# Kernel optimization log

Hardware: AMD Instinct MI355X
Metric: run time of the kernel (lower is better)

## Reference

```python
import jax, jax.numpy as jnp
import numpy as np

B, N, D_IN = 64, 512, 768
FEA, HEADS = 256, 8
NEG_SLOPE = 0.2  # GATConv default leaky_relu slope


def setup_inputs() -> dict:
    key = jax.random.key(0)
    ks = jax.random.split(key, 7)
    scale = lambda fan_in: 1.0 / np.sqrt(fan_in)
    return {
        "x": jax.random.normal(ks[0], (B, N, D_IN), dtype=jnp.float32),
        # outer LazyLinear(fea_dim) with bias
        "W1": jax.random.normal(ks[1], (D_IN, FEA), dtype=jnp.float32) * scale(D_IN),
        "b1": jnp.zeros((FEA,), dtype=jnp.float32),
        # GATConv lin: Linear(FEA, HEADS*FEA, bias=False)
        "Wg": jax.random.normal(ks[2], (FEA, HEADS * FEA), dtype=jnp.float32) * scale(FEA),
        "att_src": jax.random.normal(ks[3], (HEADS, FEA), dtype=jnp.float32) * scale(FEA),
        "att_dst": jax.random.normal(ks[4], (HEADS, FEA), dtype=jnp.float32) * scale(FEA),
        # GATConv bias (concat=False -> out_channels)
        "bias_g": jnp.zeros((FEA,), dtype=jnp.float32),
    }


def reference(x, W1, b1, Wg, att_src, att_dst, bias_g):
    # outer projection: [B,N,FEA]
    x1 = jnp.einsum("bnd,df->bnf", x, W1) + b1
    # GAT projection into heads: [B,N,H,C]
    h = jnp.einsum("bnf,fk->bnk", x1, Wg).reshape(B, N, HEADS, FEA)
    # per-node attention logits: [B,N,H]
    a_src = jnp.einsum("bnhc,hc->bnh", h, att_src)
    a_dst = jnp.einsum("bnhc,hc->bnh", h, att_dst)
    # graph is fully connected + self-loops (PyG add_self_loops=True),
    # so per-target softmax == dense softmax over all source nodes j.
    # logits[b,h,i,j] = a_dst[b,i,h] + a_src[b,j,h]
    logits = a_dst.transpose(0, 2, 1)[:, :, :, None] + a_src.transpose(0, 2, 1)[:, :, None, :]
    logits = jnp.where(logits >= 0, logits, NEG_SLOPE * logits)  # leaky_relu
    alpha = jax.nn.softmax(logits, axis=-1)  # [B,H,I,J]
    # weighted aggregation: out[b,i,h,c] = sum_j alpha[b,h,i,j] * h[b,j,h,c]
    out = jnp.einsum("bhij,bjhc->bihc", alpha, h)
    out = out.mean(axis=2) + bias_g  # concat=False -> mean over heads, [B,N,FEA]
    return out.mean(axis=1)  # mean over nodes -> [B,FEA]
```

## Files before the change

kernel.cpp:

```cpp
#include <hip/hip_runtime.h>

#define BATCH 64
#define NNODE 512
#define D_IN 768
#define FEA 256
#define HEADS 8
#define M_ROWS (BATCH * NNODE)
#define NEG_SLOPE 0.2f
#define LOG2E 1.4426950408889634f
#define JC 16

typedef __attribute__((ext_vector_type(4))) float f32x4;
typedef __attribute__((ext_vector_type(8))) short bf16x8;

__device__ __forceinline__ ushort f2bf(float f) {
    union { float f; unsigned u; } v; v.f = f;
    unsigned r = v.u + 0x7fffu + ((v.u >> 16) & 1u);
    return (ushort)(r >> 16);
}
__device__ __forceinline__ float exp2fast(float v) { return __builtin_amdgcn_exp2f(v); }

__global__ __launch_bounds__(256) void k_att_proj(const float* __restrict__ Wg,
                                                  const float* __restrict__ att_src,
                                                  const float* __restrict__ att_dst,
                                                  float* __restrict__ was,
                                                  float* __restrict__ wad) {
    int h = blockIdx.x;
    const float* a = (blockIdx.y == 0) ? att_src : att_dst;
    float* o = (blockIdx.y == 0) ? was : wad;
    int wv = threadIdx.x >> 6, lane = threadIdx.x & 63;
    float4 av = *(const float4*)&a[h * FEA + lane * 4];
    int fbase = blockIdx.z * 64 + wv;
    #pragma unroll
    for (int i = 0; i < 16; i++) {
        int f = fbase + i * 4;
        float4 g = *(const float4*)&Wg[(size_t)f * (HEADS * FEA) + h * FEA + lane * 4];
        float p = g.x * av.x + g.y * av.y + g.z * av.z + g.w * av.w;
        #pragma unroll
        for (int off = 32; off; off >>= 1) p += __shfl_xor(p, off);
        if (lane == 0) o[h * FEA + f] = p;
    }
}

__global__ __launch_bounds__(256) void k_prep_was1(const float* __restrict__ W1,
                                                   const float* __restrict__ b1,
                                                   const float* __restrict__ was,
                                                   const float* __restrict__ wad,
                                                   ushort* __restrict__ Bpk,
                                                   float* __restrict__ c_sd) {
    __shared__ float wvl[16 * 260];
    __shared__ float w1l[8][256];
    __shared__ float partial[256];
    int t = threadIdx.x;
    int blk = blockIdx.x;
    int k0 = blk * 8;
    for (int i = t; i < 4096; i += 256) {
        int col = i >> 8, f = i & 255;
        wvl[col * 260 + f] = (col < 8) ? was[col * 256 + f] : wad[(col - 8) * 256 + f];
    }
    for (int i = t; i < 2048; i += 256) {
        int r = i >> 8, c = i & 255;
        w1l[r][c] = W1[(size_t)(k0 + r) * 256 + c];
    }
    __syncthreads();
    int col = t & 15, r = (t >> 4) & 7, half = t >> 7;
    float acc = 0.f;
    const float* wr = &w1l[r][half * 128];
    const float* vr = &wvl[col * 260 + half * 128];
    #pragma unroll 4
    for (int f0 = 0; f0 < 128; f0 += 4) {
        float4 a4 = *(const float4*)&wr[f0];
        float4 v4 = *(const float4*)&vr[f0];
        acc += a4.x * v4.x + a4.y * v4.y + a4.z * v4.z + a4.w * v4.w;
    }
    partial[t] = acc;
    __syncthreads();
    if (t < 128) {
        float tot = partial[t] + partial[t + 128];
        int kt = blk >> 2;
        int kloc = (blk & 3) * 8 + r;
        Bpk[kt * 1024 + ((kloc >> 3) * 16 + col) * 8 + (kloc & 7)] = f2bf(tot);
    }
    if (blk == 0 && t < 16) {
        float a = 0.f;
        for (int f = 0; f < 256; f++) a += b1[f] * wvl[t * 260 + f];
        c_sd[t] = a;
    }
}

__global__ __launch_bounds__(256) void k_logits(const float* __restrict__ x,
                                                const ushort* __restrict__ Bpk,
                                                const float* __restrict__ c_sd,
                                                float* __restrict__ a_src,
                                                float* __restrict__ a_dst) {
    int t = threadIdx.x;
    int w = t >> 6, l = t & 63;
    int lr = l & 15, lk = l >> 4;
    int row0w = blockIdx.x * 64 + w * 16;
    const float* ap = x + (size_t)(row0w + lr) * D_IN + lk * 8;
    const ushort* bp = Bpk + l * 8;

    f32x4 A0[3], A1[3];
    bf16x8 Bf[3];
    A0[0] = *(const f32x4*)(ap);      A1[0] = *(const f32x4*)(ap + 4);
    Bf[0] = *(const bf16x8*)(bp);
    A0[1] = *(const f32x4*)(ap + 32); A1[1] = *(const f32x4*)(ap + 36);
    Bf[1] = *(const bf16x8*)(bp + 1024);
    f32x4 acc = {};

    #pragma unroll
    for (int kt = 0; kt < 24; kt++) {
        int cur = kt % 3;
        if (kt + 2 < 24) {
            int nx = (kt + 2) % 3;
            A0[nx] = *(const f32x4*)(ap + (kt + 2) * 32);
            A1[nx] = *(const f32x4*)(ap + (kt + 2) * 32 + 4);
            Bf[nx] = *(const bf16x8*)(bp + (size_t)(kt + 2) * 1024);
        }
        bf16x8 af;
        af[0] = (short)f2bf(A0[cur].x); af[1] = (short)f2bf(A0[cur].y);
        af[2] = (short)f2bf(A0[cur].z); af[3] = (short)f2bf(A0[cur].w);
        af[4] = (short)f2bf(A1[cur].x); af[5] = (short)f2bf(A1[cur].y);
        af[6] = (short)f2bf(A1[cur].z); af[7] = (short)f2bf(A1[cur].w);
        acc = __builtin_amdgcn_mfma_f32_16x16x32_bf16(af, Bf[cur], acc, 0, 0, 0);
    }
    int col = lr;
    float cadd = c_sd[col];
    float* dst = (col < 8) ? a_src : a_dst;
    int h = col & 7;
    #pragma unroll
    for (int r = 0; r < 4; r++) {
        int rr = row0w + lk * 4 + r;
        int b = rr >> 9, n = rr & 511;
        dst[((size_t)(b * 8 + h) << 9) + n] = (acc[r] + cadd) * LOG2E;
    }
}

__global__ __launch_bounds__(512) void k_softmax(const float* __restrict__ a_src,
                                                 const float* __restrict__ a_dst,
                                                 float* __restrict__ wout,
                                                 float* __restrict__ s_w) {
    __shared__ float s_srt[512], d_srt[512];
    __shared__ float E1[512], E2[512], PA[512], PB[512];
    __shared__ float red[8], tA[8], tB[8];
    int t = threadIdx.x;
    int lane = t & 63, wv = t >> 6;
    int bh = blockIdx.x;
    float sv = a_src[((size_t)bh << 9) + t];
    float dv = a_dst[((size_t)bh << 9) + t];
    float v_s = sv, v_d = dv;
    float mx = sv;
    #pragma unroll
    for (int off = 32; off; off >>= 1) mx = fmaxf(mx, __shfl_xor(mx, off));
    if (lane == 0) red[wv] = mx;
    __syncthreads();
    mx = red[0];
    #pragma unroll
    for (int k = 1; k < 8; k++) mx = fmaxf(mx, red[k]);
    for (int k = 2; k <= 512; k <<= 1) {
        for (int j = k >> 1; j > 0; j >>= 1) {
            bool lower = ((t & j) == 0);
            bool tmin = (lower == ((t & k) == 0));
            if (j >= 64) {
                __syncthreads();
                s_srt[t] = v_s; d_srt[t] = v_d;
                __syncthreads();
                float ps = s_srt[t ^ j], pd = d_srt[t ^ j];
                v_s = tmin ? fminf(v_s, ps) : fmaxf(v_s, ps);
                v_d = tmin ? fminf(v_d, pd) : fmaxf(v_d, pd);
            } else {
                float ps = __shfl_xor(v_s, j);
                float pd = __shfl_xor(v_d, j);
                v_s = tmin ? fminf(v_s, ps) : fmaxf(v_s, ps);
                v_d = tmin ? fminf(v_d, pd) : fmaxf(v_d, pd);
            }
        }
    }
    __syncthreads();
    s_srt[t] = v_s; d_srt[t] = v_d;
    float e1 = exp2fast(v_s - mx);
    float e2 = exp2fast(0.2f * (v_s - mx));
    #pragma unroll
    for (int off = 1; off < 64; off <<= 1) {
        float u1 = __shfl_up(e1, off);
        float u2 = __shfl_up(e2, off);
        if (lane >= off) { e1 += u1; e2 += u2; }
    }
    if (lane == 63) { tA[wv] = e1; tB[wv] = e2; }
    __syncthreads();
    float pre1 = 0.f, pre2 = 0.f, tot1 = 0.f, tot2 = 0.f;
    #pragma unroll
    for (int k = 0; k < 8; k++) {
        float a = tA[k], b = tB[k];
        tot1 += a; tot2 += b;
        if (k < wv) { pre1 += a; pre2 += b; }
    }
    e1 += pre1; e2 += pre2;
    E1[t] = e1; E2[t] = e2;
    __syncthreads();
    float v = v_d + mx;
    float mi = fmaxf(v, NEG_SLOPE * v);
    float key = -v_d;
    int lo = 0, hi = 512;
    #pragma unroll
    for (int it = 0; it < 9; it++) {
        if (lo < hi) {
            int mid = (lo + hi) >> 1;
            if (s_srt[mid] < key) lo = mid + 1; else hi = mid;
        }
    }
    float e1pre = lo ? E1[lo - 1] : 0.f;
    float e2pre = lo ? E2[lo - 1] : 0.f;
    float ga = exp2fast(v - mi);
    float gb = exp2fast(0.2f * v - mi);
    float L = ga * (tot1 - e1pre) + gb * e2pre;
    float linv = 1.f / L;
    float pa = ga * linv, pb = gb * linv;
    #pragma unroll
    for (int off = 1; off < 64; off <<= 1) {
        float u1 = __shfl_up(pa, off);
        float u2 = __shfl_up(pb, off);
        if (lane >= off) { pa += u1; pb += u2; }
    }
    __syncthreads();
    if (lane == 63) { tA[wv] = pa; tB[wv] = pb; }
    __syncthreads();
    float prp1 = 0.f, prp2 = 0.f, totp1 = 0.f, totp2 = 0.f;
    #pragma unroll
    for (int k = 0; k < 8; k++) {
        float a = tA[k], b = tB[k];
        totp1 += a; totp2 += b;
        if (k < wv) { prp1 += a; prp2 += b; }
    }
    pa += prp1; pb += prp2;
    PA[t] = pa; PB[t] = pb;
    __syncthreads();
    float key2 = -sv;
    int lo2 = 0, hi2 = 512;
    #pragma unroll
    for (int it = 0; it < 9; it++) {
        if (lo2 < hi2) {
            int mid = (lo2 + hi2) >> 1;
            if (d_srt[mid] < key2) lo2 = mid + 1; else hi2 = mid;
        }
    }
    float papre = lo2 ? PA[lo2 - 1] : 0.f;
    float pbpre = lo2 ? PB[lo2 - 1] : 0.f;
    float e1j = exp2fast(sv - mx);
    float e2j = exp2fast(0.2f * (sv - mx));
    float wj = e1j * (totp1 - papre) + e2j * pbpre;
    wout[((size_t)bh << 9) + t] = wj;
    float ssum = wj;
    #pragma unroll
    for (int off = 32; off; off >>= 1) ssum += __shfl_xor(ssum, off);
    __syncthreads();
    if (lane == 0) red[wv] = ssum;
    __syncthreads();
    if (t == 0) {
        float a = 0.f;
        #pragma unroll
        for (int k = 0; k < 8; k++) a += red[k];
        s_w[bh] = a;
    }
}

__global__ __launch_bounds__(192) void k_zsum(const float* __restrict__ w,
                                              const float* __restrict__ x,
                                              float* __restrict__ z_part) {
    __shared__ float wl[256];
    int t = threadIdx.x;
    int b = blockIdx.x, jc = blockIdx.y;
    for (int i = t; i < 256; i += 192) {
        int h = i >> 5, j = i & 31;
        wl[i] = w[((size_t)(b * 8 + h) << 9) + jc * 32 + j];
    }
    __syncthreads();
    f32x4 acc[8] = {};
    const float* xp = x + ((size_t)(b * 512 + jc * 32)) * D_IN + t * 4;
    for (int j = 0; j < 32; j++) {
        f32x4 xv = *(const f32x4*)(xp + (size_t)j * D_IN);
        #pragma unroll
        for (int h = 0; h < 8; h++) {
            float wv = wl[h * 32 + j];
            acc[h] = acc[h] + wv * xv;
        }
    }
    #pragma unroll
    for (int h = 0; h < 8; h++)
        *(f32x4*)&z_part[((size_t)((b * JC + jc) * 8 + h)) * D_IN + t * 4] = acc[h];
}

__global__ __launch_bounds__(256) void k_y(const float* __restrict__ z_part,
                                           const float* __restrict__ W1,
                                           const float* __restrict__ b1,
                                           const float* __restrict__ s_w,
                                           float* __restrict__ y_part) {
    __shared__ float zl[8 * 196];
    int t = threadIdx.x;
    int b = blockIdx.x, ds = blockIdx.y;
    for (int sIdx = t; sIdx < 1536; sIdx += 256) {
        int k = sIdx / 192, dd = sIdx - k * 192;
        float v = 0.f;
        #pragma unroll
        for (int jc = 0; jc < JC; jc++)
            v += z_part[((size_t)((b * JC + jc) * 8 + k)) * D_IN + ds * 192 + dd];
        zl[k * 196 + dd] = v;
    }
    __syncthreads();
    float acc[8] = {};
    for (int dq = 0; dq < 48; dq++) {
        int dbase = ds * 192 + dq * 4;
        float w0 = W1[(size_t)(dbase + 0) * 256 + t];
        float w1 = W1[(size_t)(dbase + 1) * 256 + t];
        float w2 = W1[(size_t)(dbase + 2) * 256 + t];
        float w3 = W1[(size_t)(dbase + 3) * 256 + t];
        #pragma unroll
        for (int k = 0; k < 8; k++) {
            float4 zq = *(const float4*)&zl[k * 196 + dq * 4];
            acc[k] += zq.x * w0 + zq.y * w1 + zq.z * w2 + zq.w * w3;
        }
    }
    #pragma unroll
    for (int k = 0; k < 8; k++) {
        float v = acc[k];
        if (ds == 0) v += s_w[b * 8 + k] * b1[t];
        y_part[((size_t)ds * 512 + b * 8 + k) * 256 + t] = v;
    }
}

__global__ __launch_bounds__(256) void k_out(const float* __restrict__ y_part,
                                             const float* __restrict__ Wg,
                                             float* __restrict__ out_part) {
    __shared__ float Yl[64][16];
    int t = threadIdx.x;
    int h = blockIdx.x, fs = blockIdx.y, bq = blockIdx.z;
    int f0 = fs * 64, b0 = bq * 16;
    for (int sIdx = t; sIdx < 1024; sIdx += 256) {
        int bl = sIdx >> 6, fl = sIdx & 63;
        float v = 0.f;
        #pragma unroll
        for (int ds = 0; ds < 4; ds++)
            v += y_part[((size_t)(ds * 512) + (b0 + bl) * 8 + h) * 256 + f0 + fl];
        Yl[fl][bl] = v;
    }
    __syncthreads();
    float acc[16] = {};
    for (int fl = 0; fl < 64; fl++) {
        float wv = Wg[(size_t)(f0 + fl) * 2048 + h * 256 + t];
        #pragma unroll
        for (int bl = 0; bl < 16; bl++) acc[bl] += Yl[fl][bl] * wv;
    }
    #pragma unroll
    for (int bl = 0; bl < 16; bl++)
        out_part[((size_t)(h * 4 + fs) * 64 + b0 + bl) * 256 + t] = acc[bl];
}

__global__ __launch_bounds__(256) void k_out2(const float* __restrict__ out_part,
                                              const float* __restrict__ bias_g,
                                              float* __restrict__ out) {
    int t = threadIdx.x, b = blockIdx.x;
    float acc = 0.f;
    #pragma unroll
    for (int k = 0; k < 32; k++) acc += out_part[((size_t)k * 64 + b) * 256 + t];
    out[b * 256 + t] = bias_g[t] + acc * (1.f / 4096.f);
}

extern "C" void kernel_launch(void* const* d_in, const int* in_sizes, int n_in,
                              void* d_out, int out_size, void* d_ws, size_t ws_size,
                              hipStream_t stream) {
    const float* x       = (const float*)d_in[0];
    const float* W1      = (const float*)d_in[1];
    const float* b1      = (const float*)d_in[2];
    const float* Wg      = (const float*)d_in[3];
    const float* att_src = (const float*)d_in[4];
    const float* att_dst = (const float*)d_in[5];
    const float* bias_g  = (const float*)d_in[6];
    float* out = (float*)d_out;

    float* ws       = (float*)d_ws;
    float* was      = ws;
    float* wad      = ws + 2048;
    float* c_sd     = ws + 4096;
    ushort* Bpk     = (ushort*)(ws + 4112);
    float* a_src    = ws + 16400;
    float* a_dst    = ws + 278544;
    float* wsum     = ws + 540688;
    float* s_w      = ws + 802832;
    float* z_part   = ws + 803344;
    float* y_part   = ws + 7094800;
    float* out_part = ws + 7619088;

    k_att_proj<<<dim3(HEADS, 2, 4), 256, 0, stream>>>(Wg, att_src, att_dst, was, wad);
    k_prep_was1<<<96, 256, 0, stream>>>(W1, b1, was, wad, Bpk, c_sd);
    k_logits<<<M_ROWS / 64, 256, 0, stream>>>(x, Bpk, c_sd, a_src, a_dst);
    k_softmax<<<BATCH * HEADS, 512, 0, stream>>>(a_src, a_dst, wsum, s_w);
    k_zsum<<<dim3(BATCH, JC), 192, 0, stream>>>(wsum, x, z_part);
    k_y<<<dim3(BATCH, 4), 256, 0, stream>>>(z_part, W1, b1, s_w, y_part);
    k_out<<<dim3(HEADS, 4, 4), 256, 0, stream>>>(y_part, Wg, out_part);
    k_out2<<<BATCH, 256, 0, stream>>>(out_part, bias_g, out);
}
```

Baseline: 94.40 us.

## Fuse all eight stages into one cooperative persistent kernel with grid syncs

Replaces the eight separate kernel launches with a single cooperative kernel of 256 blocks of 512 threads. Stages are separated by grid.sync, and each block handles two former 256-thread work units or two softmax rows. The z-sum stage is repartitioned from 16 chunks to 4 per batch, with an in-block reduction, which shrinks the z_part buffer. This removes launch gaps and inter-kernel drain, at the cost of grid-wide barriers and idle blocks in the small stages.

```diff
diff --git a/kernel.cpp b/kernel.cpp
--- a/kernel.cpp
+++ b/kernel.cpp
@@ -1,14 +1,10 @@
 #include <hip/hip_runtime.h>
-
-#define BATCH 64
-#define NNODE 512
-#define D_IN 768
-#define FEA 256
-#define HEADS 8
-#define M_ROWS (BATCH * NNODE)
+#include <hip/hip_cooperative_groups.h>
+
+namespace cg = cooperative_groups;
+
 #define NEG_SLOPE 0.2f
 #define LOG2E 1.4426950408889634f
-#define JC 16
 
 typedef __attribute__((ext_vector_type(4))) float f32x4;
 typedef __attribute__((ext_vector_type(8))) short bf16x8;
@@ -20,349 +16,408 @@
 }
 __device__ __forceinline__ float exp2fast(float v) { return __builtin_amdgcn_exp2f(v); }
 
-__global__ __launch_bounds__(256) void k_att_proj(const float* __restrict__ Wg,
-                                                  const float* __restrict__ att_src,
-                                                  const float* __restrict__ att_dst,
-                                                  float* __restrict__ was,
-                                                  float* __restrict__ wad) {
-    int h = blockIdx.x;
-    const float* a = (blockIdx.y == 0) ? att_src : att_dst;
-    float* o = (blockIdx.y == 0) ? was : wad;
-    int wv = threadIdx.x >> 6, lane = threadIdx.x & 63;
-    float4 av = *(const float4*)&a[h * FEA + lane * 4];
-    int fbase = blockIdx.z * 64 + wv;
-    #pragma unroll
-    for (int i = 0; i < 16; i++) {
-        int f = fbase + i * 4;
-        float4 g = *(const float4*)&Wg[(size_t)f * (HEADS * FEA) + h * FEA + lane * 4];
-        float p = g.x * av.x + g.y * av.y + g.z * av.z + g.w * av.w;
-        #pragma unroll
-        for (int off = 32; off; off >>= 1) p += __shfl_xor(p, off);
-        if (lane == 0) o[h * FEA + f] = p;
-    }
-}
-
-__global__ __launch_bounds__(256) void k_prep_was1(const float* __restrict__ W1,
-                                                   const float* __restrict__ b1,
-                                                   const float* __restrict__ was,
-                                                   const float* __restrict__ wad,
-                                                   ushort* __restrict__ Bpk,
-                                                   float* __restrict__ c_sd) {
-    __shared__ float wvl[16 * 260];
-    __shared__ float w1l[8][256];
-    __shared__ float partial[256];
-    int t = threadIdx.x;
-    int blk = blockIdx.x;
-    int k0 = blk * 8;
-    for (int i = t; i < 4096; i += 256) {
-        int col = i >> 8, f = i & 255;
-        wvl[col * 260 + f] = (col < 8) ? was[col * 256 + f] : wad[(col - 8) * 256 + f];
-    }
-    for (int i = t; i < 2048; i += 256) {
-        int r = i >> 8, c = i & 255;
-        w1l[r][c] = W1[(size_t)(k0 + r) * 256 + c];
-    }
-    __syncthreads();
-    int col = t & 15, r = (t >> 4) & 7, half = t >> 7;
-    float acc = 0.f;
-    const float* wr = &w1l[r][half * 128];
-    const float* vr = &wvl[col * 260 + half * 128];
-    #pragma unroll 4
-    for (int f0 = 0; f0 < 128; f0 += 4) {
-        float4 a4 = *(const float4*)&wr[f0];
-        float4 v4 = *(const float4*)&vr[f0];
-        acc += a4.x * v4.x + a4.y * v4.y + a4.z * v4.z + a4.w * v4.w;
-    }
-    partial[t] = acc;
-    __syncthreads();
-    if (t < 128) {
-        float tot = partial[t] + partial[t + 128];
-        int kt = blk >> 2;
-        int kloc = (blk & 3) * 8 + r;
-        Bpk[kt * 1024 + ((kloc >> 3) * 16 + col) * 8 + (kloc & 7)] = f2bf(tot);
-    }
-    if (blk == 0 && t < 16) {
-        float a = 0.f;
-        for (int f = 0; f < 256; f++) a += b1[f] * wvl[t * 260 + f];
-        c_sd[t] = a;
-    }
-}
-
-__global__ __launch_bounds__(256) void k_logits(const float* __restrict__ x,
-                                                const ushort* __restrict__ Bpk,
-                                                const float* __restrict__ c_sd,
-                                                float* __restrict__ a_src,
-                                                float* __restrict__ a_dst) {
-    int t = threadIdx.x;
-    int w = t >> 6, l = t & 63;
-    int lr = l & 15, lk = l >> 4;
-    int row0w = blockIdx.x * 64 + w * 16;
-    const float* ap = x + (size_t)(row0w + lr) * D_IN + lk * 8;
-    const ushort* bp = Bpk + l * 8;
-
-    f32x4 A0[3], A1[3];
-    bf16x8 Bf[3];
-    A0[0] = *(const f32x4*)(ap);      A1[0] = *(const f32x4*)(ap + 4);
-    Bf[0] = *(const bf16x8*)(bp);
-    A0[1] = *(const f32x4*)(ap + 32); A1[1] = *(const f32x4*)(ap + 36);
-    Bf[1] = *(const bf16x8*)(bp + 1024);
-    f32x4 acc = {};
-
-    #pragma unroll
-    for (int kt = 0; kt < 24; kt++) {
-        int cur = kt % 3;
-        if (kt + 2 < 24) {
-            int nx = (kt + 2) % 3;
-            A0[nx] = *(const f32x4*)(ap + (kt + 2) * 32);
-            A1[nx] = *(const f32x4*)(ap + (kt + 2) * 32 + 4);
-            Bf[nx] = *(const bf16x8*)(bp + (size_t)(kt + 2) * 1024);
-        }
-        bf16x8 af;
-        af[0] = (short)f2bf(A0[cur].x); af[1] = (short)f2bf(A0[cur].y);
-        af[2] = (short)f2bf(A0[cur].z); af[3] = (short)f2bf(A0[cur].w);
-        af[4] = (short)f2bf(A1[cur].x); af[5] = (short)f2bf(A1[cur].y);
-        af[6] = (short)f2bf(A1[cur].z); af[7] = (short)f2bf(A1[cur].w);
-        acc = __builtin_amdgcn_mfma_f32_16x16x32_bf16(af, Bf[cur], acc, 0, 0, 0);
-    }
-    int col = lr;
-    float cadd = c_sd[col];
-    float* dst = (col < 8) ? a_src : a_dst;
-    int h = col & 7;
-    #pragma unroll
-    for (int r = 0; r < 4; r++) {
-        int rr = row0w + lk * 4 + r;
-        int b = rr >> 9, n = rr & 511;
-        dst[((size_t)(b * 8 + h) << 9) + n] = (acc[r] + cadd) * LOG2E;
-    }
-}
-
-__global__ __launch_bounds__(512) void k_softmax(const float* __restrict__ a_src,
-                                                 const float* __restrict__ a_dst,
-                                                 float* __restrict__ wout,
-                                                 float* __restrict__ s_w) {
-    __shared__ float s_srt[512], d_srt[512];
-    __shared__ float E1[512], E2[512], PA[512], PB[512];
-    __shared__ float red[8], tA[8], tB[8];
-    int t = threadIdx.x;
-    int lane = t & 63, wv = t >> 6;
-    int bh = blockIdx.x;
-    float sv = a_src[((size_t)bh << 9) + t];
-    float dv = a_dst[((size_t)bh << 9) + t];
-    float v_s = sv, v_d = dv;
-    float mx = sv;
-    #pragma unroll
-    for (int off = 32; off; off >>= 1) mx = fmaxf(mx, __shfl_xor(mx, off));
-    if (lane == 0) red[wv] = mx;
-    __syncthreads();
-    mx = red[0];
-    #pragma unroll
-    for (int k = 1; k < 8; k++) mx = fmaxf(mx, red[k]);
-    for (int k = 2; k <= 512; k <<= 1) {
-        for (int j = k >> 1; j > 0; j >>= 1) {
-            bool lower = ((t & j) == 0);
-            bool tmin = (lower == ((t & k) == 0));
-            if (j >= 64) {
-                __syncthreads();
-                s_srt[t] = v_s; d_srt[t] = v_d;
-                __syncthreads();
-                float ps = s_srt[t ^ j], pd = d_srt[t ^ j];
-                v_s = tmin ? fminf(v_s, ps) : fmaxf(v_s, ps);
-                v_d = tmin ? fminf(v_d, pd) : fmaxf(v_d, pd);
-            } else {
-                float ps = __shfl_xor(v_s, j);
-                float pd = __shfl_xor(v_d, j);
-                v_s = tmin ? fminf(v_s, ps) : fmaxf(v_s, ps);
-                v_d = tmin ? fminf(v_d, pd) : fmaxf(v_d, pd);
-            }
-        }
-    }
-    __syncthreads();
-    s_srt[t] = v_s; d_srt[t] = v_d;
-    float e1 = exp2fast(v_s - mx);
-    float e2 = exp2fast(0.2f * (v_s - mx));
-    #pragma unroll
-    for (int off = 1; off < 64; off <<= 1) {
-        float u1 = __shfl_up(e1, off);
-        float u2 = __shfl_up(e2, off);
-        if (lane >= off) { e1 += u1; e2 += u2; }
-    }
-    if (lane == 63) { tA[wv] = e1; tB[wv] = e2; }
-    __syncthreads();
-    float pre1 = 0.f, pre2 = 0.f, tot1 = 0.f, tot2 = 0.f;
-    #pragma unroll
-    for (int k = 0; k < 8; k++) {
-        float a = tA[k], b = tB[k];
-        tot1 += a; tot2 += b;
-        if (k < wv) { pre1 += a; pre2 += b; }
-    }
-    e1 += pre1; e2 += pre2;
-    E1[t] = e1; E2[t] = e2;
-    __syncthreads();
-    float v = v_d + mx;
-    float mi = fmaxf(v, NEG_SLOPE * v);
-    float key = -v_d;
-    int lo = 0, hi = 512;
-    #pragma unroll
-    for (int it = 0; it < 9; it++) {
-        if (lo < hi) {
-            int mid = (lo + hi) >> 1;
-            if (s_srt[mid] < key) lo = mid + 1; else hi = mid;
-        }
-    }
-    float e1pre = lo ? E1[lo - 1] : 0.f;
-    float e2pre = lo ? E2[lo - 1] : 0.f;
-    float ga = exp2fast(v - mi);
-    float gb = exp2fast(0.2f * v - mi);
-    float L = ga * (tot1 - e1pre) + gb * e2pre;
-    float linv = 1.f / L;
-    float pa = ga * linv, pb = gb * linv;
-    #pragma unroll
-    for (int off = 1; off < 64; off <<= 1) {
-        float u1 = __shfl_up(pa, off);
-        float u2 = __shfl_up(pb, off);
-        if (lane >= off) { pa += u1; pb += u2; }
-    }
-    __syncthreads();
-    if (lane == 63) { tA[wv] = pa; tB[wv] = pb; }
-    __syncthreads();
-    float prp1 = 0.f, prp2 = 0.f, totp1 = 0.f, totp2 = 0.f;
-    #pragma unroll
-    for (int k = 0; k < 8; k++) {
-        float a = tA[k], b = tB[k];
-        totp1 += a; totp2 += b;
-        if (k < wv) { prp1 += a; prp2 += b; }
-    }
-    pa += prp1; pb += prp2;
-    PA[t] = pa; PB[t] = pb;
-    __syncthreads();
-    float key2 = -sv;
-    int lo2 = 0, hi2 = 512;
-    #pragma unroll
-    for (int it = 0; it < 9; it++) {
-        if (lo2 < hi2) {
-            int mid = (lo2 + hi2) >> 1;
-            if (d_srt[mid] < key2) lo2 = mid + 1; else hi2 = mid;
-        }
-    }
-    float papre = lo2 ? PA[lo2 - 1] : 0.f;
-    float pbpre = lo2 ? PB[lo2 - 1] : 0.f;
-    float e1j = exp2fast(sv - mx);
-    float e2j = exp2fast(0.2f * (sv - mx));
-    float wj = e1j * (totp1 - papre) + e2j * pbpre;
-    wout[((size_t)bh << 9) + t] = wj;
-    float ssum = wj;
-    #pragma unroll
-    for (int off = 32; off; off >>= 1) ssum += __shfl_xor(ssum, off);
-    __syncthreads();
-    if (lane == 0) red[wv] = ssum;
-    __syncthreads();
-    if (t == 0) {
-        float a = 0.f;
-        #pragma unroll
-        for (int k = 0; k < 8; k++) a += red[k];
-        s_w[bh] = a;
-    }
-}
-
-__global__ __launch_bounds__(192) void k_zsum(const float* __restrict__ w,
-                                              const float* __restrict__ x,
-                                              float* __restrict__ z_part) {
-    __shared__ float wl[256];
-    int t = threadIdx.x;
-    int b = blockIdx.x, jc = blockIdx.y;
-    for (int i = t; i < 256; i += 192) {
-        int h = i >> 5, j = i & 31;
-        wl[i] = w[((size_t)(b * 8 + h) << 9) + jc * 32 + j];
-    }
-    __syncthreads();
-    f32x4 acc[8] = {};
-    const float* xp = x + ((size_t)(b * 512 + jc * 32)) * D_IN + t * 4;
-    for (int j = 0; j < 32; j++) {
-        f32x4 xv = *(const f32x4*)(xp + (size_t)j * D_IN);
-        #pragma unroll
-        for (int h = 0; h < 8; h++) {
-            float wv = wl[h * 32 + j];
-            acc[h] = acc[h] + wv * xv;
-        }
-    }
-    #pragma unroll
-    for (int h = 0; h < 8; h++)
-        *(f32x4*)&z_part[((size_t)((b * JC + jc) * 8 + h)) * D_IN + t * 4] = acc[h];
-}
-
-__global__ __launch_bounds__(256) void k_y(const float* __restrict__ z_part,
-                                           const float* __restrict__ W1,
-                                           const float* __restrict__ b1,
-                                           const float* __restrict__ s_w,
-                                           float* __restrict__ y_part) {
-    __shared__ float zl[8 * 196];
-    int t = threadIdx.x;
-    int b = blockIdx.x, ds = blockIdx.y;
-    for (int sIdx = t; sIdx < 1536; sIdx += 256) {
-        int k = sIdx / 192, dd = sIdx - k * 192;
-        float v = 0.f;
-        #pragma unroll
-        for (int jc = 0; jc < JC; jc++)
-            v += z_part[((size_t)((b * JC + jc) * 8 + k)) * D_IN + ds * 192 + dd];
-        zl[k * 196 + dd] = v;
-    }
-    __syncthreads();
-    float acc[8] = {};
-    for (int dq = 0; dq < 48; dq++) {
-        int dbase = ds * 192 + dq * 4;
-        float w0 = W1[(size_t)(dbase + 0) * 256 + t];
-        float w1 = W1[(size_t)(dbase + 1) * 256 + t];
-        float w2 = W1[(size_t)(dbase + 2) * 256 + t];
-        float w3 = W1[(size_t)(dbase + 3) * 256 + t];
+__global__ __launch_bounds__(512) void k_mega(
+    const float* __restrict__ x, const float* __restrict__ W1, const float* __restrict__ b1,
+    const float* __restrict__ Wg, const float* __restrict__ att_src, const float* __restrict__ att_dst,
+    const float* __restrict__ bias_g, float* __restrict__ out,
+    float* __restrict__ was, float* __restrict__ wad, float* __restrict__ c_sd,
+    ushort* __restrict__ Bpk, float* __restrict__ a_src, float* __restrict__ a_dst,
+    float* __restrict__ wsum, float* __restrict__ s_w, float* __restrict__ z_part,
+    float* __restrict__ y_part, float* __restrict__ out_part)
+{
+    __shared__ float smem[12928];
+    cg::grid_group grid = cg::this_grid();
+    const int t = threadIdx.x;
+    const int blk = blockIdx.x;
+    const int half = t >> 8;
+    const int tl = t & 255;
+
+    if (blk < 32) {
+        int u = blk * 2 + half;
+        int h = u & 7;
+        const float* a = ((u >> 3) & 1) ? att_dst : att_src;
+        float* o = ((u >> 3) & 1) ? wad : was;
+        int z4 = u >> 4;
+        int wv = tl >> 6, lane = tl & 63;
+        float4 av = *(const float4*)&a[h * 256 + lane * 4];
+        int fbase = z4 * 64 + wv;
+        #pragma unroll
+        for (int i = 0; i < 16; i++) {
+            int f = fbase + i * 4;
+            float4 g = *(const float4*)&Wg[(size_t)f * 2048 + h * 256 + lane * 4];
+            float p = g.x * av.x + g.y * av.y + g.z * av.z + g.w * av.w;
+            #pragma unroll
+            for (int off = 32; off; off >>= 1) p += __shfl_xor(p, off);
+            if (lane == 0) o[h * 256 + f] = p;
+        }
+    }
+    grid.sync();
+
+    if (blk < 48) {
+        int unit = blk * 2 + half;
+        float* wvl = smem + half * 6464;
+        float* w1l = wvl + 4160;
+        float* partial = w1l + 2048;
+        for (int i = tl; i < 4096; i += 256) {
+            int col = i >> 8, f = i & 255;
+            wvl[col * 260 + f] = (col < 8) ? was[col * 256 + f] : wad[(col - 8) * 256 + f];
+        }
+        int k0 = unit * 8;
+        for (int i = tl; i < 2048; i += 256) {
+            int r = i >> 8, c = i & 255;
+            w1l[r * 256 + c] = W1[(size_t)(k0 + r) * 256 + c];
+        }
+        __syncthreads();
+        int col = tl & 15, r = (tl >> 4) & 7, hh = tl >> 7;
+        float acc = 0.f;
+        const float* wr = &w1l[r * 256 + hh * 128];
+        const float* vr = &wvl[col * 260 + hh * 128];
+        #pragma unroll 4
+        for (int f0 = 0; f0 < 128; f0 += 4) {
+            float4 a4 = *(const float4*)&wr[f0];
+            float4 v4 = *(const float4*)&vr[f0];
+            acc += a4.x * v4.x + a4.y * v4.y + a4.z * v4.z + a4.w * v4.w;
+        }
+        partial[tl] = acc;
+        __syncthreads();
+        if (tl < 128) {
+            float tot = partial[tl] + partial[tl + 128];
+            int kt = unit >> 2;
+            int kloc = (unit & 3) * 8 + r;
+            Bpk[kt * 1024 + ((kloc >> 3) * 16 + col) * 8 + (kloc & 7)] = f2bf(tot);
+        }
+        if (unit == 0 && tl < 16) {
+            float a = 0.f;
+            for (int f = 0; f < 256; f++) a += b1[f] * wvl[tl * 260 + f];
+            c_sd[tl] = a;
+        }
+    }
+    grid.sync();
+
+    {
+        int unit = blk * 2 + half;
+        int w = tl >> 6, l = tl & 63;
+        int lr = l & 15, lk = l >> 4;
+        int row0w = unit * 64 + w * 16;
+        const float* ap = x + (size_t)(row0w + lr) * 768 + lk * 8;
+        const ushort* bp = Bpk + l * 8;
+
+        f32x4 A0[3], A1[3];
+        bf16x8 Bf[3];
+        A0[0] = *(const f32x4*)(ap);      A1[0] = *(const f32x4*)(ap + 4);
+        Bf[0] = *(const bf16x8*)(bp);
+        A0[1] = *(const f32x4*)(ap + 32); A1[1] = *(const f32x4*)(ap + 36);
+        Bf[1] = *(const bf16x8*)(bp + 1024);
+        f32x4 acc = {};
+        #pragma unroll
+        for (int kt = 0; kt < 24; kt++) {
+            int cur = kt % 3;
+            if (kt + 2 < 24) {
+                int nx = (kt + 2) % 3;
+                A0[nx] = *(const f32x4*)(ap + (kt + 2) * 32);
+                A1[nx] = *(const f32x4*)(ap + (kt + 2) * 32 + 4);
+                Bf[nx] = *(const bf16x8*)(bp + (size_t)(kt + 2) * 1024);
+            }
+            bf16x8 af;
+            af[0] = (short)f2bf(A0[cur].x); af[1] = (short)f2bf(A0[cur].y);
+            af[2] = (short)f2bf(A0[cur].z); af[3] = (short)f2bf(A0[cur].w);
+            af[4] = (short)f2bf(A1[cur].x); af[5] = (short)f2bf(A1[cur].y);
+            af[6] = (short)f2bf(A1[cur].z); af[7] = (short)f2bf(A1[cur].w);
+            acc = __builtin_amdgcn_mfma_f32_16x16x32_bf16(af, Bf[cur], acc, 0, 0, 0);
+        }
+        int col = lr;
+        float cadd = c_sd[col];
+        float* dst = (col < 8) ? a_src : a_dst;
+        int h = col & 7;
+        #pragma unroll
+        for (int r = 0; r < 4; r++) {
+            int rr = row0w + lk * 4 + r;
+            int b = rr >> 9, n = rr & 511;
+            dst[((size_t)(b * 8 + h) << 9) + n] = (acc[r] + cadd) * LOG2E;
+        }
+    }
+    grid.sync();
+
+    {
+        float* Ss = smem;
+        float* Ds = smem + 1024;
+        float* E1 = smem + 2048;
+        float* E2 = smem + 3072;
+        float* PAa = smem + 4096;
+        float* PBa = smem + 5120;
+        float* red = smem + 6144;
+        float* tAa = smem + 6160;
+        float* tBa = smem + 6176;
+        int lane = t & 63, wv8 = t >> 6;
+        int bh0 = blk * 2;
+        float sv[2], dv[2], vs[2], vd[2], mx[2];
+        #pragma unroll
+        for (int u = 0; u < 2; u++) {
+            sv[u] = a_src[((size_t)(bh0 + u) << 9) + t];
+            dv[u] = a_dst[((size_t)(bh0 + u) << 9) + t];
+            vs[u] = sv[u]; vd[u] = dv[u]; mx[u] = sv[u];
+        }
+        #pragma unroll
+        for (int off = 32; off; off >>= 1) {
+            mx[0] = fmaxf(mx[0], __shfl_xor(mx[0], off));
+            mx[1] = fmaxf(mx[1], __shfl_xor(mx[1], off));
+        }
+        if (lane == 0) { red[wv8] = mx[0]; red[8 + wv8] = mx[1]; }
+        __syncthreads();
+        #pragma unroll
+        for (int u = 0; u < 2; u++) {
+            float m = red[u * 8];
+            #pragma unroll
+            for (int k = 1; k < 8; k++) m = fmaxf(m, red[u * 8 + k]);
+            mx[u] = m;
+        }
+        for (int k = 2; k <= 512; k <<= 1) {
+            for (int j = k >> 1; j > 0; j >>= 1) {
+                bool tmin = (((t & j) == 0) == ((t & k) == 0));
+                if (j >= 64) {
+                    __syncthreads();
+                    Ss[t] = vs[0]; Ss[512 + t] = vs[1];
+                    Ds[t] = vd[0]; Ds[512 + t] = vd[1];
+                    __syncthreads();
+                    float p0 = Ss[t ^ j], p1 = Ss[512 + (t ^ j)];
+                    float q0 = Ds[t ^ j], q1 = Ds[512 + (t ^ j)];
+                    vs[0] = tmin ? fminf(vs[0], p0) : fmaxf(vs[0], p0);
+                    vs[1] = tmin ? fminf(vs[1], p1) : fmaxf(vs[1], p1);
+                    vd[0] = tmin ? fminf(vd[0], q0) : fmaxf(vd[0], q0);
+                    vd[1] = tmin ? fminf(vd[1], q1) : fmaxf(vd[1], q1);
+                } else {
+                    float p0 = __shfl_xor(vs[0], j), p1 = __shfl_xor(vs[1], j);
+                    float q0 = __shfl_xor(vd[0], j), q1 = __shfl_xor(vd[1], j);
+                    vs[0] = tmin ? fminf(vs[0], p0) : fmaxf(vs[0], p0);
+                    vs[1] = tmin ? fminf(vs[1], p1) : fmaxf(vs[1], p1);
+                    vd[0] = tmin ? fminf(vd[0], q0) : fmaxf(vd[0], q0);
+                    vd[1] = tmin ? fminf(vd[1], q1) : fmaxf(vd[1], q1);
+                }
+            }
+        }
+        __syncthreads();
+        Ss[t] = vs[0]; Ss[512 + t] = vs[1];
+        Ds[t] = vd[0]; Ds[512 + t] = vd[1];
+        float e1[2], e2[2];
+        #pragma unroll
+        for (int u = 0; u < 2; u++) {
+            e1[u] = exp2fast(vs[u] - mx[u]);
+            e2[u] = exp2fast(0.2f * (vs[u] - mx[u]));
+        }
+        #pragma unroll
+        for (int off = 1; off < 64; off <<= 1) {
+            float u10 = __shfl_up(e1[0], off), u11 = __shfl_up(e1[1], off);
+            float u20 = __shfl_up(e2[0], off), u21 = __shfl_up(e2[1], off);
+            if (lane >= off) { e1[0] += u10; e1[1] += u11; e2[0] += u20; e2[1] += u21; }
+        }
+        if (lane == 63) {
+            tAa[wv8] = e1[0]; tAa[8 + wv8] = e1[1];
+            tBa[wv8] = e2[0]; tBa[8 + wv8] = e2[1];
+        }
+        __syncthreads();
+        float tot1[2], tot2[2];
+        #pragma unroll
+        for (int u = 0; u < 2; u++) {
+            float p1 = 0.f, p2 = 0.f, s1 = 0.f, s2 = 0.f;
+            #pragma unroll
+            for (int k = 0; k < 8; k++) {
+                float a = tAa[u * 8 + k], b = tBa[u * 8 + k];
+                s1 += a; s2 += b;
+                if (k < wv8) { p1 += a; p2 += b; }
+            }
+            e1[u] += p1; e2[u] += p2; tot1[u] = s1; tot2[u] = s2;
+            E1[u * 512 + t] = e1[u]; E2[u * 512 + t] = e2[u];
+        }
+        __syncthreads();
+        float pa[2], pb[2];
+        #pragma unroll
+        for (int u = 0; u < 2; u++) {
+            float v = vd[u] + mx[u];
+            float mi = fmaxf(v, NEG_SLOPE * v);
+            float key = -vd[u];
+            int lo = 0, hi = 512;
+            #pragma unroll
+            for (int it = 0; it < 9; it++) {
+                if (lo < hi) {
+                    int mid = (lo + hi) >> 1;
+                    if (Ss[u * 512 + mid] < key) lo = mid + 1; else hi = mid;
+                }
+            }
+            float e1pre = lo ? E1[u * 512 + lo - 1] : 0.f;
+            float e2pre = lo ? E2[u * 512 + lo - 1] : 0.f;
+            float ga = exp2fast(v - mi);
+            float gb = exp2fast(0.2f * v - mi);
+            float L = ga * (tot1[u] - e1pre) + gb * e2pre;
+            float linv = 1.f / L;
+            pa[u] = ga * linv; pb[u] = gb * linv;
+        }
+        #pragma unroll
+        for (int off = 1; off < 64; off <<= 1) {
+            float u10 = __shfl_up(pa[0], off), u11 = __shfl_up(pa[1], off);
+            float u20 = __shfl_up(pb[0], off), u21 = __shfl_up(pb[1], off);
+            if (lane >= off) { pa[0] += u10; pa[1] += u11; pb[0] += u20; pb[1] += u21; }
+        }
+        if (lane == 63) {
+            tAa[wv8] = pa[0]; tAa[8 + wv8] = pa[1];
+            tBa[wv8] = pb[0]; tBa[8 + wv8] = pb[1];
+        }
+        __syncthreads();
+        float totp1[2], totp2[2];
+        #pragma unroll
+        for (int u = 0; u < 2; u++) {
+            float p1 = 0.f, p2 = 0.f, s1 = 0.f, s2 = 0.f;
+            #pragma unroll
+            for (int k = 0; k < 8; k++) {
+                float a = tAa[u * 8 + k], b = tBa[u * 8 + k];
+                s1 += a; s2 += b;
+                if (k < wv8) { p1 += a; p2 += b; }
+            }
+            pa[u] += p1; pb[u] += p2; totp1[u] = s1; totp2[u] = s2;
+            PAa[u * 512 + t] = pa[u]; PBa[u * 512 + t] = pb[u];
+        }
+        __syncthreads();
+        float ssum[2];
+        #pragma unroll
+        for (int u = 0; u < 2; u++) {
+            float key2 = -sv[u];
+            int lo2 = 0, hi2 = 512;
+            #pragma unroll
+            for (int it = 0; it < 9; it++) {
+                if (lo2 < hi2) {
+                    int mid = (lo2 + hi2) >> 1;
+                    if (Ds[u * 512 + mid] < key2) lo2 = mid + 1; else hi2 = mid;
+                }
+            }
+            float papre = lo2 ? PAa[u * 512 + lo2 - 1] : 0.f;
+            float pbpre = lo2 ? PBa[u * 512 + lo2 - 1] : 0.f;
+            float e1j = exp2fast(sv[u] - mx[u]);
+            float e2j = exp2fast(0.2f * (sv[u] - mx[u]));
+            float wj = e1j * (totp1[u] - papre) + e2j * pbpre;
+            wsum[((size_t)(bh0 + u) << 9) + t] = wj;
+            ssum[u] = wj;
+        }
+        #pragma unroll
+        for (int off = 32; off; off >>= 1) {
+            ssum[0] += __shfl_xor(ssum[0], off);
+            ssum[1] += __shfl_xor(ssum[1], off);
+        }
+        __syncthreads();
+        if (lane == 0) { red[wv8] = ssum[0]; red[8 + wv8] = ssum[1]; }
+        __syncthreads();
+        if (t == 0) {
+            float a0 = 0.f, a1 = 0.f;
+            #pragma unroll
+            for (int k = 0; k < 8; k++) { a0 += red[k]; a1 += red[8 + k]; }
+            s_w[bh0] = a0; s_w[bh0 + 1] = a1;
+        }
+    }
+    grid.sync();
+
+    {
+        int b = blk >> 2, q = blk & 3;
+        float* wl = smem;
+        float* cb = smem + 1024;
+        for (int i = t; i < 1024; i += 512) {
+            int h = i >> 7, j = i & 127;
+            wl[i] = wsum[((size_t)(b * 8 + h) << 9) + q * 128 + j];
+        }
+        __syncthreads();
+        int jh = t / 192, col = t % 192;
+        f32x4 acc[8] = {};
+        if (t < 384) {
+            const float* xp = x + ((size_t)(b * 512 + q * 128 + jh * 64)) * 768 + col * 4;
+            for (int j = 0; j < 64; j++) {
+                f32x4 xv = *(const f32x4*)(xp + (size_t)j * 768);
+                #pragma unroll
+                for (int h = 0; h < 8; h++) {
+                    float wv = wl[h * 128 + jh * 64 + j];
+                    acc[h] += wv * xv;
+                }
+            }
+            if (jh == 1) {
+                #pragma unroll
+                for (int h = 0; h < 8; h++) *(f32x4*)&cb[(h * 192 + col) * 4] = acc[h];
+            }
+        }
+        __syncthreads();
+        if (jh == 0) {
+            #pragma unroll
+            for (int h = 0; h < 8; h++) {
+                acc[h] += *(const f32x4*)&cb[(h * 192 + col) * 4];
+                *(f32x4*)&z_part[((size_t)((b * 4 + q) * 8 + h)) * 768 + col * 4] = acc[h];
+            }
+        }
+    }
+    grid.sync();
+
+    if (blk < 128) {
+        int unit = blk * 2 + half;
+        int b = unit >> 2, ds = unit & 3;
+        float* zl = smem + half * 1600;
+        for (int sIdx = tl; sIdx < 1536; sIdx += 256) {
+            int k = sIdx / 192, dd = sIdx - k * 192;
+            float v = 0.f;
+            #pragma unroll
+            for (int jc = 0; jc < 4; jc++)
+                v += z_part[((size_t)((b * 4 + jc) * 8 + k)) * 768 + ds * 192 + dd];
+            zl[k * 196 + dd] = v;
+        }
+        __syncthreads();
+        float acc[8] = {};
+        for (int dq = 0; dq < 48; dq++) {
+            int dbase = ds * 192 + dq * 4;
+            float w0 = W1[(size_t)(dbase + 0) * 256 + tl];
+            float w1 = W1[(size_t)(dbase + 1) * 256 + tl];
+            float w2 = W1[(size_t)(dbase + 2) * 256 + tl];
+            float w3 = W1[(size_t)(dbase + 3) * 256 + tl];
+            #pragma unroll
+            for (int k = 0; k < 8; k++) {
+                float4 zq = *(const float4*)&zl[k * 196 + dq * 4];
+                acc[k] += zq.x * w0 + zq.y * w1 + zq.z * w2 + zq.w * w3;
+            }
+        }
         #pragma unroll
         for (int k = 0; k < 8; k++) {
-            float4 zq = *(const float4*)&zl[k * 196 + dq * 4];
-            acc[k] += zq.x * w0 + zq.y * w1 + zq.z * w2 + zq.w * w3;
-        }
-    }
-    #pragma unroll
-    for (int k = 0; k < 8; k++) {
-        float v = acc[k];
-        if (ds == 0) v += s_w[b * 8 + k] * b1[t];
-        y_part[((size_t)ds * 512 + b * 8 + k) * 256 + t] = v;
-    }
-}
-
-__global__ __launch_bounds__(256) void k_out(const float* __restrict__ y_part,
-                                             const float* __restrict__ Wg,
-                                             float* __restrict__ out_part) {
-    __shared__ float Yl[64][16];
-    int t = threadIdx.x;
-    int h = blockIdx.x, fs = blockIdx.y, bq = blockIdx.z;
-    int f0 = fs * 64, b0 = bq * 16;
-    for (int sIdx = t; sIdx < 1024; sIdx += 256) {
-        int bl = sIdx >> 6, fl = sIdx & 63;
-        float v = 0.f;
-        #pragma unroll
-        for (int ds = 0; ds < 4; ds++)
-            v += y_part[((size_t)(ds * 512) + (b0 + bl) * 8 + h) * 256 + f0 + fl];
-        Yl[fl][bl] = v;
-    }
-    __syncthreads();
-    float acc[16] = {};
-    for (int fl = 0; fl < 64; fl++) {
-        float wv = Wg[(size_t)(f0 + fl) * 2048 + h * 256 + t];
-        #pragma unroll
-        for (int bl = 0; bl < 16; bl++) acc[bl] += Yl[fl][bl] * wv;
-    }
-    #pragma unroll
-    for (int bl = 0; bl < 16; bl++)
-        out_part[((size_t)(h * 4 + fs) * 64 + b0 + bl) * 256 + t] = acc[bl];
-}
-
-__global__ __launch_bounds__(256) void k_out2(const float* __restrict__ out_part,
-                                              const float* __restrict__ bias_g,
-                                              float* __restrict__ out) {
-    int t = threadIdx.x, b = blockIdx.x;
-    float acc = 0.f;
-    #pragma unroll
-    for (int k = 0; k < 32; k++) acc += out_part[((size_t)k * 64 + b) * 256 + t];
-    out[b * 256 + t] = bias_g[t] + acc * (1.f / 4096.f);
+            float v = acc[k];
+            if (ds == 0) v += s_w[b * 8 + k] * b1[tl];
+            y_part[((size_t)ds * 512 + b * 8 + k) * 256 + tl] = v;
+        }
+    }
+    grid.sync();
+
+    if (blk < 64) {
+        int unit = blk * 2 + half;
+        int h = unit >> 4, fs = (unit >> 2) & 3, bq = unit & 3;
+        float* Yl = smem + half * 1024;
+        int f0 = fs * 64, b0 = bq * 16;
+        for (int sIdx = tl; sIdx < 1024; sIdx += 256) {
+            int bl = sIdx >> 6, fl = sIdx & 63;
+            float v = 0.f;
+            #pragma unroll
+            for (int ds = 0; ds < 4; ds++)
+                v += y_part[((size_t)(ds * 512) + (b0 + bl) * 8 + h) * 256 + f0 + fl];
+            Yl[fl * 16 + bl] = v;
+        }
+        __syncthreads();
+        float acc[16] = {};
+        for (int fl = 0; fl < 64; fl++) {
+            float wv = Wg[(size_t)(f0 + fl) * 2048 + h * 256 + tl];
+            #pragma unroll
+            for (int bl = 0; bl < 16; bl++) acc[bl] += Yl[fl * 16 + bl] * wv;
+        }
+        #pragma unroll
+        for (int bl = 0; bl < 16; bl++)
+            out_part[((size_t)(h * 4 + fs) * 64 + b0 + bl) * 256 + tl] = acc[bl];
+    }
+    grid.sync();
+
+    if (blk < 32) {
+        int b = blk * 2 + half;
+        float acc = 0.f;
+        #pragma unroll
+        for (int k2 = 0; k2 < 32; k2++) acc += out_part[((size_t)k2 * 64 + b) * 256 + tl];
+        out[b * 256 + tl] = bias_g[tl] + acc * (1.f / 4096.f);
+    }
 }
 
 extern "C" void kernel_launch(void* const* d_in, const int* in_sizes, int n_in,
@@ -387,15 +442,14 @@
     float* wsum     = ws + 540688;
     float* s_w      = ws + 802832;
     float* z_part   = ws + 803344;
-    float* y_part   = ws + 7094800;
-    float* out_part = ws + 7619088;
-
-    k_att_proj<<<dim3(HEADS, 2, 4), 256, 0, stream>>>(Wg, att_src, att_dst, was, wad);
-    k_prep_was1<<<96, 256, 0, stream>>>(W1, b1, was, wad, Bpk, c_sd);
-    k_logits<<<M_ROWS / 64, 256, 0, stream>>>(x, Bpk, c_sd, a_src, a_dst);
-    k_softmax<<<BATCH * HEADS, 512, 0, stream>>>(a_src, a_dst, wsum, s_w);
-    k_zsum<<<dim3(BATCH, JC), 192, 0, stream>>>(wsum, x, z_part);
-    k_y<<<dim3(BATCH, 4), 256, 0, stream>>>(z_part, W1, b1, s_w, y_part);
-    k_out<<<dim3(HEADS, 4, 4), 256, 0, stream>>>(y_part, Wg, out_part);
-    k_out2<<<BATCH, 256, 0, stream>>>(out_part, bias_g, out);
+    float* y_part   = ws + 2376208;
+    float* out_part = ws + 2900496;
+
+    void* args[] = {
+        (void*)&x, (void*)&W1, (void*)&b1, (void*)&Wg, (void*)&att_src, (void*)&att_dst,
+        (void*)&bias_g, (void*)&out, (void*)&was, (void*)&wad, (void*)&c_sd, (void*)&Bpk,
+        (void*)&a_src, (void*)&a_dst, (void*)&wsum, (void*)&s_w, (void*)&z_part,
+        (void*)&y_part, (void*)&out_part
+    };
+    hipLaunchCooperativeKernel((const void*)k_mega, dim3(256), dim3(512), args, 0, stream);
 }
```

Result: slower. 292.2 us (+209.5%).
